# Kernel optimization log

Hardware: AMD Instinct MI355X
Metric: run time of the kernel (lower is better)

## Reference

```python
import jax, jax.numpy as jnp
import numpy as np

H = 1024      # hidden_size
V = 32000     # output_size (vocab)
L = 512       # max_length (encoder positions)
B = 256       # batch


def setup_inputs() -> dict:
    key = jax.random.key(0)
    ks = jax.random.split(key, 12)
    s = 0.02
    return {
        "input": jax.random.randint(ks[0], (B,), 0, V),
        "hidden": jax.random.normal(ks[1], (1, B, H), jnp.float32),
        "encoder_outputs": jax.random.normal(ks[2], (L, H), jnp.float32),
        # learned params (PyTorch layout: Linear weight is [out, in])
        "emb": jax.random.normal(ks[3], (V, H), jnp.float32) * s,
        "attn_W": jax.random.normal(ks[4], (L, 2 * H), jnp.float32) * s,
        "attn_b": jnp.zeros((L,), jnp.float32),
        "comb_W": jax.random.normal(ks[5], (H, 2 * H), jnp.float32) * s,
        "comb_b": jnp.zeros((H,), jnp.float32),
        "W_ih": jax.random.normal(ks[6], (3 * H, H), jnp.float32) * s,
        "W_hh": jax.random.normal(ks[7], (3 * H, H), jnp.float32) * s,
        "b_ih": jnp.zeros((3 * H,), jnp.float32),
        "b_hh": jnp.zeros((3 * H,), jnp.float32),
        "out_W": jax.random.normal(ks[8], (V, H), jnp.float32) * s,
        "out_b": jnp.zeros((V,), jnp.float32),
    }


def reference(input, hidden, encoder_outputs, emb, attn_W, attn_b,
              comb_W, comb_b, W_ih, W_hh, b_ih, b_hh, out_W, out_b):
    h = hidden[0]                                   # [B,H]
    embedded = emb[input]                           # [B,H] (dropout in eval mode = identity)
    attn_logits = jnp.concatenate([embedded, h], axis=1) @ attn_W.T + attn_b
    attn_weights = jax.nn.softmax(attn_logits, axis=1)        # [B,L]
    attn_applied = attn_weights @ encoder_outputs              # [B,H]
    x = jnp.concatenate([embedded, attn_applied], axis=1) @ comb_W.T + comb_b
    x = jax.nn.relu(x)                                         # [B,H]
    # single-step GRU (PyTorch gate layout: r, z, n)
    gi = x @ W_ih.T + b_ih                                     # [B,3H]
    gh = h @ W_hh.T + b_hh                                     # [B,3H]
    gi_r, gi_z, gi_n = jnp.split(gi, 3, axis=1)
    gh_r, gh_z, gh_n = jnp.split(gh, 3, axis=1)
    r = jax.nn.sigmoid(gi_r + gh_r)
    z = jax.nn.sigmoid(gi_z + gh_z)
    n = jnp.tanh(gi_n + r * gh_n)
    h_new = (1.0 - z) * n + z * h                              # [B,H]
    output = jax.nn.log_softmax(h_new @ out_W.T + out_b, axis=1)  # [B,V]
    return output, h_new[None], attn_weights
```

## Files before the change

kernel.cpp:

```cpp
#include <hip/hip_runtime.h>
#include <hip/hip_bf16.h>
#include <cstdint>

#define DEVI __device__ __forceinline__

typedef __bf16 bf16x8 __attribute__((ext_vector_type(8)));
typedef float  f32x4  __attribute__((ext_vector_type(4)));

constexpr int Hdim = 1024;
constexpr int Vdim = 32000;
constexpr int Ldim = 512;
constexpr int Bdim = 256;

DEVI unsigned short f2bf(float f) {
  __bf16 h = (__bf16)f;
  return __builtin_bit_cast(unsigned short, h);
}

constexpr int FP4 = 36;

__global__ __launch_bounds__(1024, 4)
void gemm_flat5(const unsigned short* __restrict__ A,
                const float* __restrict__ W,
                const float* __restrict__ bias,
                float* __restrict__ C,
                float2* __restrict__ plse)
{
  __shared__ unsigned short lW[4][128 * FP4];

  const int t    = threadIdx.x;
  const int lane = t & 63;
  const int wv   = t >> 6;
  const int r16  = lane & 15;
  const int k8   = (lane >> 4) * 8;
  const int n0   = blockIdx.x * 128;

  const int srow = t >> 3;
  const int stc  = (t & 7) * 4;

  const float*          Wb = W + (size_t)(n0 + srow) * 1024 + stc;
  const unsigned short* Ab = A + (size_t)(wv * 16 + r16) * 1024 + k8;

  f32x4 acc[8];
#pragma unroll
  for (int n = 0; n < 8; ++n)
#pragma unroll
    for (int r = 0; r < 4; ++r) acc[n][r] = 0.f;

  f32x4 w0_, w1_;
  uint4 a0_, a1_, a2_, a3_;

#define LOADW(RW, KT) RW = *reinterpret_cast<const f32x4*>(Wb + (KT) * 32)
#define LOADA(RA, KT) RA = *reinterpret_cast<const uint4*>(Ab + (KT) * 32)

#define STOREW(RW, BUF) do {                                                   \
    ushort4 u_;                                                                \
    u_.x = f2bf(RW[0]); u_.y = f2bf(RW[1]);                                    \
    u_.z = f2bf(RW[2]); u_.w = f2bf(RW[3]);                                    \
    *reinterpret_cast<ushort4*>(&lW[BUF][srow * FP4 + stc]) = u_;              \
  } while (0)

#define COMP(RA, BUF) do {                                                     \
    _Pragma("unroll")                                                          \
    for (int n = 0; n < 8; ++n) {                                              \
      bf16x8 bw_ = *reinterpret_cast<const bf16x8*>(                           \
          &lW[BUF][(n * 16 + r16) * FP4 + k8]);                                \
      acc[n] = __builtin_amdgcn_mfma_f32_16x16x32_bf16(                        \
          __builtin_bit_cast(bf16x8, RA), bw_, acc[n], 0, 0, 0);               \
    }                                                                          \
  } while (0)

  LOADW(w0_, 0); LOADW(w1_, 1);
  LOADA(a0_, 0); LOADA(a1_, 1); LOADA(a2_, 2); LOADA(a3_, 3);
  STOREW(w0_, 0); LOADW(w0_, 2);
  STOREW(w1_, 1); LOADW(w1_, 3);
  __syncthreads();

  for (int kt = 0; kt < 32; kt += 4) {
    COMP(a0_, 0);
    STOREW(w0_, 2);
    { const int kn = (kt + 4 < 32) ? kt + 4 : 31; LOADW(w0_, kn); LOADA(a0_, kn); }
    __syncthreads();

    COMP(a1_, 1);
    STOREW(w1_, 3);
    { const int kn = (kt + 5 < 32) ? kt + 5 : 31; LOADW(w1_, kn); LOADA(a1_, kn); }
    __syncthreads();

    COMP(a2_, 2);
    STOREW(w0_, 0);
    { const int kn = (kt + 6 < 32) ? kt + 6 : 31; LOADW(w0_, kn); LOADA(a2_, kn); }
    __syncthreads();

    COMP(a3_, 3);
    STOREW(w1_, 1);
    { const int kn = (kt + 7 < 32) ? kt + 7 : 31; LOADW(w1_, kn); LOADA(a3_, kn); }
    __syncthreads();
  }

#undef COMP
#undef STOREW
#undef LOADA
#undef LOADW

#pragma unroll
  for (int n = 0; n < 8; ++n) {
    const int col = n0 + n * 16 + r16;
    const float bv = bias[col];
    const int rbase = wv * 16 + (lane >> 4) * 4;
#pragma unroll
    for (int r = 0; r < 4; ++r) {
      const float v = acc[n][r] + bv;
      acc[n][r] = v;
      C[(size_t)(rbase + r) * Vdim + col] = v;
    }
  }
#pragma unroll
  for (int r = 0; r < 4; ++r) {
    float mx = -1e30f;
#pragma unroll
    for (int n = 0; n < 8; ++n) mx = fmaxf(mx, acc[n][r]);
#pragma unroll
    for (int o = 1; o < 16; o <<= 1) mx = fmaxf(mx, __shfl_xor(mx, o, 16));
    float s = 0.f;
#pragma unroll
    for (int n = 0; n < 8; ++n) s += __expf(acc[n][r] - mx);
#pragma unroll
    for (int o = 1; o < 16; o <<= 1) s += __shfl_xor(s, o, 16);
    if (r16 == 0) {
      const int row = wv * 16 + (lane >> 4) * 4 + r;
      plse[(size_t)row * gridDim.x + blockIdx.x] = make_float2(mx, s);
    }
  }
}

template<int WM, bool ABF16, bool DUAL>
__global__ __launch_bounds__(256, 2)
void gemm_bt(const void* __restrict__ Av0, const float* __restrict__ Wt0,
             const void* __restrict__ Av1, const float* __restrict__ Wt1,
             const float* __restrict__ bias,
             float* __restrict__ C0, float* __restrict__ C1,
             int K, int ldc, int col_off, int act, int aact0,
             int nsplit)
{
  constexpr int MT    = 4 * WM;
  constexpr int PITCH = 40;
  constexpr int ITA   = MT / 32;
  constexpr int MR    = WM / 16;

  __shared__ unsigned short lA[2 * MT * PITCH];
  __shared__ unsigned short lW[2 * 64 * PITCH];

  const int t  = threadIdx.x;
  const int m0 = blockIdx.y * MT;
  const int n0 = blockIdx.x * 64;

  int kz = blockIdx.z, half = 0;
  if (DUAL) { half = (kz >= nsplit) ? 1 : 0; kz -= half * nsplit; }
  const int NK = K / (32 * nsplit);
  const int kb = kz * NK;

  const void*  Av = (DUAL && half) ? Av1 : Av0;
  const float* Wt = (DUAL && half) ? Wt1 : Wt0;
  float*       C  = (DUAL && half) ? C1  : C0;
  const int  aact = (DUAL && half) ? 0 : aact0;

  const int tr = t >> 3;
  const int tc = (t & 7) * 4;

  const float*          Af = ABF16 ? nullptr : ((const float*)Av) + (size_t)m0 * K;
  const unsigned short* Ab = ABF16 ? ((const unsigned short*)Av) + (size_t)m0 * K : nullptr;
  const float*          Wb = Wt + (size_t)n0 * K;

  const int lane = t & 63;
  const int wv   = t >> 6;
  const int r16  = lane & 15;
  const int k8   = (lane >> 4) * 8;

  f32x4 acc[MR][4];
#pragma unroll
  for (int m = 0; m < MR; ++m)
#pragma unroll
    for (int n = 0; n < 4; ++n)
#pragma unroll
      for (int r = 0; r < 4; ++r) acc[m][n][r] = 0.f;

  struct RS { f32x4 ra[ITA]; ushort4 rab[ITA]; f32x4 rw[2]; };

  auto loadT = [&](RS& rg, int kt) {
    const int ko = (kb + kt) * 32 + tc;
    if constexpr (ABF16) {
      const unsigned short* ap = Ab + ko;
#pragma unroll
      for (int i = 0; i < ITA; ++i)
        rg.rab[i] = *reinterpret_cast<const ushort4*>(ap + (size_t)(tr + 32 * i) * K);
    } else {
      const float* ap = Af + ko;
#pragma unroll
      for (int i = 0; i < ITA; ++i)
        rg.ra[i] = *reinterpret_cast<const f32x4*>(ap + (size_t)(tr + 32 * i) * K);
    }
    const float* wp = Wb + ko;
#pragma unroll
    for (int i = 0; i < 2; ++i)
      rg.rw[i] = *reinterpret_cast<const f32x4*>(wp + (size_t)(tr + 32 * i) * K);
  };

  auto storeT = [&](RS& rg, int bo) {
    unsigned short* sA = &lA[bo * MT * PITCH];
    unsigned short* sW = &lW[bo * 64 * PITCH];
#pragma unroll
    for (int i = 0; i < ITA; ++i) {
      ushort4 u;
      if constexpr (ABF16) u = rg.rab[i];
      else {
        f32x4 v = rg.ra[i];
        if (aact) { v[0]=fmaxf(v[0],0.f); v[1]=fmaxf(v[1],0.f);
                    v[2]=fmaxf(v[2],0.f); v[3]=fmaxf(v[3],0.f); }
        u.x = f2bf(v[0]); u.y = f2bf(v[1]); u.z = f2bf(v[2]); u.w = f2bf(v[3]);
      }
      *reinterpret_cast<ushort4*>(&sA[(tr + 32 * i) * PITCH + tc]) = u;
    }
#pragma unroll
    for (int i = 0; i < 2; ++i) {
      f32x4 v = rg.rw[i]; ushort4 u;
      u.x = f2bf(v[0]); u.y = f2bf(v[1]); u.z = f2bf(v[2]); u.w = f2bf(v[3]);
      *reinterpret_cast<ushort4*>(&sW[(tr + 32 * i) * PITCH + tc]) = u;
    }
  };

  auto comp = [&](int bo) {
    const unsigned short* sA = &lA[bo * MT * PITCH];
    const unsigned short* sW = &lW[bo * 64 * PITCH];
    bf16x8 af[MR], bfr[4];
#pragma unroll
    for (int m = 0; m < MR; ++m)
      af[m] = *reinterpret_cast<const bf16x8*>(&sA[(wv * WM + m * 16 + r16) * PITCH + k8]);
#pragma unroll
    for (int n = 0; n < 4; ++n)
      bfr[n] = *reinterpret_cast<const bf16x8*>(&sW[(n * 16 + r16) * PITCH + k8]);
#pragma unroll
    for (int m = 0; m < MR; ++m)
#pragma unroll
      for (int n = 0; n < 4; ++n)
        acc[m][n] = __builtin_amdgcn_mfma_f32_16x16x32_bf16(af[m], bfr[n], acc[m][n], 0, 0, 0);
  };

#define GB_BARRIER() do { \
    asm volatile("s_waitcnt lgkmcnt(0)" ::: "memory"); \
    __builtin_amdgcn_sched_barrier(0); \
    __builtin_amdgcn_s_barrier(); \
  } while (0)

  RS ra_, rb_;
  loadT(ra_, 0);
  loadT(rb_, 1);
  storeT(ra_, 0);
  GB_BARRIER();

  for (int kt = 0; kt < NK; kt += 2) {
    if (kt + 2 < NK) loadT(ra_, kt + 2);
    comp(0);
    storeT(rb_, 1);
    GB_BARRIER();
    if (kt + 3 < NK) loadT(rb_, kt + 3);
    comp(1);
    if (kt + 2 < NK) {
      storeT(ra_, 0);
      GB_BARRIER();
    }
  }
#undef GB_BARRIER

#pragma unroll
  for (int n = 0; n < 4; ++n) {
    const int col = n0 + n * 16 + r16;
    const float bv = (bias && nsplit == 1) ? bias[col] : 0.f;
#pragma unroll
    for (int m = 0; m < MR; ++m) {
      const int rbase = m0 + wv * WM + m * 16 + (lane >> 4) * 4;
#pragma unroll
      for (int r = 0; r < 4; ++r) {
        float v = acc[m][n][r] + bv;
        if (act) v = fmaxf(v, 0.f);
        if (nsplit > 1) {
          atomicAdd(&C[(size_t)(rbase + r) * ldc + col_off + col], v);
        } else {
          C[(size_t)(rbase + r) * ldc + col_off + col] = v;
        }
      }
    }
  }
}

__global__ void prep_kernel(const int* __restrict__ ids, const float* __restrict__ hid,
                            const float* __restrict__ emb,
                            const float* __restrict__ attn_b, const float* __restrict__ comb_b,
                            const float* __restrict__ b_ih, const float* __restrict__ b_hh,
                            float* __restrict__ X0, float* __restrict__ X1,
                            float* __restrict__ alog, float* __restrict__ xact,
                            float* __restrict__ gi, float* __restrict__ gh)
{
  const int b = blockIdx.x, t = threadIdx.x;
  const int row = ids[b];
  f32x4 e = *reinterpret_cast<const f32x4*>(emb + (size_t)row * Hdim + t * 4);
  *reinterpret_cast<f32x4*>(X0 + (size_t)b * 2048 + t * 4) = e;
  *reinterpret_cast<f32x4*>(X1 + (size_t)b * 2048 + t * 4) = e;
  f32x4 h = *reinterpret_cast<const f32x4*>(hid + (size_t)b * Hdim + t * 4);
  *reinterpret_cast<f32x4*>(X0 + (size_t)b * 2048 + 1024 + t * 4) = h;
  f32x4 z4 = {0.f, 0.f, 0.f, 0.f};
  *reinterpret_cast<f32x4*>(X1 + (size_t)b * 2048 + 1024 + t * 4) = z4;
  if (t < 128)
    *reinterpret_cast<f32x4*>(alog + (size_t)b * Ldim + t * 4) =
        *reinterpret_cast<const f32x4*>(attn_b + t * 4);
  *reinterpret_cast<f32x4*>(xact + (size_t)b * Hdim + t * 4) =
      *reinterpret_cast<const f32x4*>(comb_b + t * 4);
#pragma unroll
  for (int i = 0; i < 3; ++i) {
    *reinterpret_cast<f32x4*>(gi + (size_t)b * 3072 + i * 1024 + t * 4) =
        *reinterpret_cast<const f32x4*>(b_ih + i * 1024 + t * 4);
    *reinterpret_cast<f32x4*>(gh + (size_t)b * 3072 + i * 1024 + t * 4) =
        *reinterpret_cast<const f32x4*>(b_hh + i * 1024 + t * 4);
  }
}

__global__ void transpose_kernel(const float* __restrict__ enc, float* __restrict__ encT)
{
  __shared__ float tile[64][65];
  const int l0 = blockIdx.x * 64, h0 = blockIdx.y * 64;
  const int t = threadIdx.x;
  const int c = t & 63, rr = t >> 6;
#pragma unroll
  for (int p = 0; p < 16; ++p) {
    const int r = p * 4 + rr;
    tile[r][c] = enc[(size_t)(l0 + r) * Hdim + h0 + c];
  }
  __syncthreads();
#pragma unroll
  for (int p = 0; p < 16; ++p) {
    const int r = p * 4 + rr;
    encT[(size_t)(h0 + r) * Ldim + l0 + c] = tile[c][r];
  }
}

__global__ void attn_softmax_kernel(const float* __restrict__ logits, float* __restrict__ wout)
{
  __shared__ float red[256];
  const int b = blockIdx.x, t = threadIdx.x;
  const float x0 = logits[b * Ldim + t];
  const float x1 = logits[b * Ldim + 256 + t];
  red[t] = fmaxf(x0, x1); __syncthreads();
  for (int o = 128; o > 0; o >>= 1) { if (t < o) red[t] = fmaxf(red[t], red[t + o]); __syncthreads(); }
  const float m = red[0]; __syncthreads();
  const float e0 = __expf(x0 - m), e1 = __expf(x1 - m);
  red[t] = e0 + e1; __syncthreads();
  for (int o = 128; o > 0; o >>= 1) { if (t < o) red[t] += red[t + o]; __syncthreads(); }
  const float inv = 1.f / red[0];
  wout[b * Ldim + t]       = e0 * inv;
  wout[b * Ldim + 256 + t] = e1 * inv;
}

DEVI float sigm(float x) { return 1.f / (1.f + __expf(-x)); }

__global__ void gru_kernel(const float* __restrict__ gi, const float* __restrict__ gh,
                           const float* __restrict__ hin,
                           float* __restrict__ hnew, unsigned short* __restrict__ hnbf)
{
  const int idx = blockIdx.x * 256 + threadIdx.x;
  const int b = idx >> 10, j = idx & 1023;
  const float* gib = gi + (size_t)b * 3072;
  const float* ghb = gh + (size_t)b * 3072;
  const float r = sigm(gib[j] + ghb[j]);
  const float z = sigm(gib[1024 + j] + ghb[1024 + j]);
  const float n = tanhf(gib[2048 + j] + r * ghb[2048 + j]);
  const float h = hin[idx];
  const float hn = (1.f - z) * n + z * h;
  hnew[idx] = hn;
  hnbf[idx] = f2bf(hn);
}

__global__ void lse_reduce(const float2* __restrict__ part, int npart,
                           float* __restrict__ lse)
{
  __shared__ float rm[256], rs[256];
  const int b = blockIdx.x, t = threadIdx.x;
  float m = -1e30f, s = 0.f;
  for (int j = t; j < npart; j += 256) {
    const float2 p = part[(size_t)b * npart + j];
    const float nm = fmaxf(m, p.x);
    s = s * __expf(m - nm) + p.y * __expf(p.x - nm);
    m = nm;
  }
  rm[t] = m; rs[t] = s; __syncthreads();
  for (int o = 128; o > 0; o >>= 1) {
    if (t < o) {
      const float m2 = rm[t + o], s2 = rs[t + o];
      const float nm = fmaxf(rm[t], m2);
      rs[t] = rs[t] * __expf(rm[t] - nm) + s2 * __expf(m2 - nm);
      rm[t] = nm;
    }
    __syncthreads();
  }
  if (t == 0) lse[b] = rm[0] + __logf(rs[0]);
}

__global__ void lsm_sub(const float* __restrict__ lse, float* __restrict__ out)
{
  const int b = blockIdx.x >> 3, c = blockIdx.x & 7;
  const float l = lse[b];
  f32x4* row4 = reinterpret_cast<f32x4*>(out + (size_t)b * Vdim) + c * 1000;
  for (int i = threadIdx.x; i < 1000; i += 256) {
    f32x4 x = row4[i];
    x[0] -= l; x[1] -= l; x[2] -= l; x[3] -= l;
    row4[i] = x;
  }
}

extern "C" void kernel_launch(void* const* d_in, const int* in_sizes, int n_in,
                              void* d_out, int out_size, void* d_ws, size_t ws_size,
                              hipStream_t stream)
{
  (void)in_sizes; (void)n_in; (void)out_size; (void)ws_size;

  const int*   ids    = (const int*)  d_in[0];
  const float* hid    = (const float*)d_in[1];
  const float* enc    = (const float*)d_in[2];
  const float* emb    = (const float*)d_in[3];
  const float* attn_W = (const float*)d_in[4];
  const float* attn_b = (const float*)d_in[5];
  const float* comb_W = (const float*)d_in[6];
  const float* comb_b = (const float*)d_in[7];
  const float* W_ih   = (const float*)d_in[8];
  const float* W_hh   = (const float*)d_in[9];
  const float* b_ih   = (const float*)d_in[10];
  const float* b_hh   = (const float*)d_in[11];
  const float* out_W  = (const float*)d_in[12];
  const float* out_b  = (const float*)d_in[13];

  float* out_logits = (float*)d_out;
  float* out_h      = out_logits + (size_t)Bdim * Vdim;
  float* out_attw   = out_h + (size_t)Bdim * Hdim;

  char* w = (char*)d_ws;
  float* X0   = (float*)w; w += (size_t)Bdim * 2048 * 4;
  float* X1   = (float*)w; w += (size_t)Bdim * 2048 * 4;
  float* encT = (float*)w; w += (size_t)Hdim * Ldim * 4;
  float* alog = (float*)w; w += (size_t)Bdim * Ldim * 4;
  float* xact = (float*)w; w += (size_t)Bdim * Hdim * 4;
  float* gi   = (float*)w; w += (size_t)Bdim * 3 * Hdim * 4;
  float* gh   = (float*)w; w += (size_t)Bdim * 3 * Hdim * 4;
  unsigned short* hnbf = (unsigned short*)w; w += (size_t)Bdim * Hdim * 2;
  float2* plse = (float2*)w; w += (size_t)Bdim * (Vdim / 32) * 8;
  float* lse  = (float*)w; w += (size_t)Bdim * 4;

  prep_kernel<<<Bdim, 256, 0, stream>>>(ids, hid, emb, attn_b, comb_b, b_ih, b_hh,
                                        X0, X1, alog, xact, gi, gh);
  transpose_kernel<<<dim3(Ldim / 64, Hdim / 64), 256, 0, stream>>>(enc, encT);

  gemm_bt<32, false, false><<<dim3(Ldim / 64, 2, 8), 256, 0, stream>>>(
      X0, attn_W, nullptr, nullptr, nullptr, alog, nullptr,
      2048, Ldim, 0, 0, 0, 8);
  attn_softmax_kernel<<<Bdim, 256, 0, stream>>>(alog, out_attw);

  gemm_bt<32, false, false><<<dim3(Hdim / 64, 2, 4), 256, 0, stream>>>(
      out_attw, encT, nullptr, nullptr, nullptr, X1, nullptr,
      512, 2048, 1024, 0, 0, 4);

  gemm_bt<32, false, false><<<dim3(Hdim / 64, 2, 8), 256, 0, stream>>>(
      X1, comb_W, nullptr, nullptr, nullptr, xact, nullptr,
      2048, Hdim, 0, 0, 0, 8);

  gemm_bt<32, false, true><<<dim3(3 * Hdim / 64, 2, 8), 256, 0, stream>>>(
      xact, W_ih, hid, W_hh, nullptr, gi, gh,
      1024, 3 * Hdim, 0, 0, 1, 4);

  gru_kernel<<<Bdim * Hdim / 256, 256, 0, stream>>>(gi, gh, hid, out_h, hnbf);

  gemm_flat5<<<Vdim / 128, 1024, 0, stream>>>(hnbf, out_W, out_b, out_logits, plse);

  lse_reduce<<<Bdim, 256, 0, stream>>>(plse, Vdim / 128, lse);
  lsm_sub<<<Bdim * 8, 256, 0, stream>>>(lse, out_logits);
}
```

Before: 122.0 us.

## Merge independent GEMMs into grouped launches and drop encoder transpose kernel

Replaces the templated split-K GEMM with a grouped kernel that takes two problem descriptors. This runs the attention-logit GEMM and the hidden-state W_hh GEMM in one launch, and moves the W_hh half out of the later dual launch. Encoder outputs are now read directly with a transposed-B load path instead of a separate transpose kernel, and the LSE reduce is fused into the log-softmax subtraction. The goal is fewer launches and less extra memory traffic. In exchange, every 8-block row group redundantly recomputes the LSE reduction, and the transposed-B LDS stores are scalar 2-byte writes that may cause bank conflicts.

```diff
diff --git a/kernel.cpp b/kernel.cpp
--- a/kernel.cpp
+++ b/kernel.cpp
@@ -134,43 +134,38 @@
   }
 }
 
-template<int WM, bool ABF16, bool DUAL>
+struct GP {
+  const float* A; const float* W; float* C;
+  int K, ldc, ldb, col_off, aact, nsplit, gx;
+};
+
+template<bool BTRANS>
 __global__ __launch_bounds__(256, 2)
-void gemm_bt(const void* __restrict__ Av0, const float* __restrict__ Wt0,
-             const void* __restrict__ Av1, const float* __restrict__ Wt1,
-             const float* __restrict__ bias,
-             float* __restrict__ C0, float* __restrict__ C1,
-             int K, int ldc, int col_off, int act, int aact0,
-             int nsplit)
-{
-  constexpr int MT    = 4 * WM;
-  constexpr int PITCH = 40;
-  constexpr int ITA   = MT / 32;
-  constexpr int MR    = WM / 16;
+void gemm_multi(GP q0, GP q1, int n0blk)
+{
+  constexpr int MT = 128, PITCH = 40, ITA = 4, MR = 2;
 
   __shared__ unsigned short lA[2 * MT * PITCH];
   __shared__ unsigned short lW[2 * 64 * PITCH];
 
+  GP p = q0;
+  int id = blockIdx.x;
+  if (id >= n0blk) { p = q1; id -= n0blk; }
+  const int bx  = id % p.gx;
+  const int rem = id / p.gx;
+  const int by  = rem & 1;
+  const int kz  = rem >> 1;
+
+  const int m0 = by * MT;
+  const int n0 = bx * 64;
+  const int NK = p.K / (32 * p.nsplit);
+  const int kb = kz * NK;
+
   const int t  = threadIdx.x;
-  const int m0 = blockIdx.y * MT;
-  const int n0 = blockIdx.x * 64;
-
-  int kz = blockIdx.z, half = 0;
-  if (DUAL) { half = (kz >= nsplit) ? 1 : 0; kz -= half * nsplit; }
-  const int NK = K / (32 * nsplit);
-  const int kb = kz * NK;
-
-  const void*  Av = (DUAL && half) ? Av1 : Av0;
-  const float* Wt = (DUAL && half) ? Wt1 : Wt0;
-  float*       C  = (DUAL && half) ? C1  : C0;
-  const int  aact = (DUAL && half) ? 0 : aact0;
-
   const int tr = t >> 3;
   const int tc = (t & 7) * 4;
 
-  const float*          Af = ABF16 ? nullptr : ((const float*)Av) + (size_t)m0 * K;
-  const unsigned short* Ab = ABF16 ? ((const unsigned short*)Av) + (size_t)m0 * K : nullptr;
-  const float*          Wb = Wt + (size_t)n0 * K;
+  const float* Af = p.A + (size_t)m0 * p.K;
 
   const int lane = t & 63;
   const int wv   = t >> 6;
@@ -185,25 +180,24 @@
 #pragma unroll
       for (int r = 0; r < 4; ++r) acc[m][n][r] = 0.f;
 
-  struct RS { f32x4 ra[ITA]; ushort4 rab[ITA]; f32x4 rw[2]; };
+  struct RS { f32x4 ra[ITA]; f32x4 rw[2]; };
 
   auto loadT = [&](RS& rg, int kt) {
-    const int ko = (kb + kt) * 32 + tc;
-    if constexpr (ABF16) {
-      const unsigned short* ap = Ab + ko;
-#pragma unroll
-      for (int i = 0; i < ITA; ++i)
-        rg.rab[i] = *reinterpret_cast<const ushort4*>(ap + (size_t)(tr + 32 * i) * K);
+    const int ko = (kb + kt) * 32;
+#pragma unroll
+    for (int i = 0; i < ITA; ++i)
+      rg.ra[i] = *reinterpret_cast<const f32x4*>(
+          Af + (size_t)(tr + 32 * i) * p.K + ko + tc);
+    if constexpr (BTRANS) {
+      const float* wp = p.W + (size_t)(ko + tr) * p.ldb + n0 + (t & 7) * 8;
+      rg.rw[0] = *reinterpret_cast<const f32x4*>(wp);
+      rg.rw[1] = *reinterpret_cast<const f32x4*>(wp + 4);
     } else {
-      const float* ap = Af + ko;
-#pragma unroll
-      for (int i = 0; i < ITA; ++i)
-        rg.ra[i] = *reinterpret_cast<const f32x4*>(ap + (size_t)(tr + 32 * i) * K);
-    }
-    const float* wp = Wb + ko;
-#pragma unroll
-    for (int i = 0; i < 2; ++i)
-      rg.rw[i] = *reinterpret_cast<const f32x4*>(wp + (size_t)(tr + 32 * i) * K);
+#pragma unroll
+      for (int i = 0; i < 2; ++i)
+        rg.rw[i] = *reinterpret_cast<const f32x4*>(
+            p.W + (size_t)(n0 + tr + 32 * i) * p.ldb + ko + tc);
+    }
   };
 
   auto storeT = [&](RS& rg, int bo) {
@@ -211,21 +205,27 @@
     unsigned short* sW = &lW[bo * 64 * PITCH];
 #pragma unroll
     for (int i = 0; i < ITA; ++i) {
+      f32x4 v = rg.ra[i];
+      if (p.aact) { v[0]=fmaxf(v[0],0.f); v[1]=fmaxf(v[1],0.f);
+                    v[2]=fmaxf(v[2],0.f); v[3]=fmaxf(v[3],0.f); }
       ushort4 u;
-      if constexpr (ABF16) u = rg.rab[i];
-      else {
-        f32x4 v = rg.ra[i];
-        if (aact) { v[0]=fmaxf(v[0],0.f); v[1]=fmaxf(v[1],0.f);
-                    v[2]=fmaxf(v[2],0.f); v[3]=fmaxf(v[3],0.f); }
+      u.x = f2bf(v[0]); u.y = f2bf(v[1]); u.z = f2bf(v[2]); u.w = f2bf(v[3]);
+      *reinterpret_cast<ushort4*>(&sA[(tr + 32 * i) * PITCH + tc]) = u;
+    }
+    if constexpr (BTRANS) {
+      const int hb = (t & 7) * 8;
+#pragma unroll
+      for (int j = 0; j < 4; ++j) {
+        sW[(hb + j)     * PITCH + tr] = f2bf(rg.rw[0][j]);
+        sW[(hb + 4 + j) * PITCH + tr] = f2bf(rg.rw[1][j]);
+      }
+    } else {
+#pragma unroll
+      for (int i = 0; i < 2; ++i) {
+        f32x4 v = rg.rw[i]; ushort4 u;
         u.x = f2bf(v[0]); u.y = f2bf(v[1]); u.z = f2bf(v[2]); u.w = f2bf(v[3]);
+        *reinterpret_cast<ushort4*>(&sW[(tr + 32 * i) * PITCH + tc]) = u;
       }
-      *reinterpret_cast<ushort4*>(&sA[(tr + 32 * i) * PITCH + tc]) = u;
-    }
-#pragma unroll
-    for (int i = 0; i < 2; ++i) {
-      f32x4 v = rg.rw[i]; ushort4 u;
-      u.x = f2bf(v[0]); u.y = f2bf(v[1]); u.z = f2bf(v[2]); u.w = f2bf(v[3]);
-      *reinterpret_cast<ushort4*>(&sW[(tr + 32 * i) * PITCH + tc]) = u;
     }
   };
 
@@ -235,7 +235,7 @@
     bf16x8 af[MR], bfr[4];
 #pragma unroll
     for (int m = 0; m < MR; ++m)
-      af[m] = *reinterpret_cast<const bf16x8*>(&sA[(wv * WM + m * 16 + r16) * PITCH + k8]);
+      af[m] = *reinterpret_cast<const bf16x8*>(&sA[(wv * 32 + m * 16 + r16) * PITCH + k8]);
 #pragma unroll
     for (int n = 0; n < 4; ++n)
       bfr[n] = *reinterpret_cast<const bf16x8*>(&sW[(n * 16 + r16) * PITCH + k8]);
@@ -275,20 +275,13 @@
 #pragma unroll
   for (int n = 0; n < 4; ++n) {
     const int col = n0 + n * 16 + r16;
-    const float bv = (bias && nsplit == 1) ? bias[col] : 0.f;
 #pragma unroll
     for (int m = 0; m < MR; ++m) {
-      const int rbase = m0 + wv * WM + m * 16 + (lane >> 4) * 4;
-#pragma unroll
-      for (int r = 0; r < 4; ++r) {
-        float v = acc[m][n][r] + bv;
-        if (act) v = fmaxf(v, 0.f);
-        if (nsplit > 1) {
-          atomicAdd(&C[(size_t)(rbase + r) * ldc + col_off + col], v);
-        } else {
-          C[(size_t)(rbase + r) * ldc + col_off + col] = v;
-        }
-      }
+      const int rbase = m0 + wv * 32 + m * 16 + (lane >> 4) * 4;
+#pragma unroll
+      for (int r = 0; r < 4; ++r)
+        atomicAdd(&p.C[(size_t)(rbase + r) * p.ldc + p.col_off + col],
+                  acc[m][n][r]);
     }
   }
 }
@@ -324,25 +317,6 @@
   }
 }
 
-__global__ void transpose_kernel(const float* __restrict__ enc, float* __restrict__ encT)
-{
-  __shared__ float tile[64][65];
-  const int l0 = blockIdx.x * 64, h0 = blockIdx.y * 64;
-  const int t = threadIdx.x;
-  const int c = t & 63, rr = t >> 6;
-#pragma unroll
-  for (int p = 0; p < 16; ++p) {
-    const int r = p * 4 + rr;
-    tile[r][c] = enc[(size_t)(l0 + r) * Hdim + h0 + c];
-  }
-  __syncthreads();
-#pragma unroll
-  for (int p = 0; p < 16; ++p) {
-    const int r = p * 4 + rr;
-    encT[(size_t)(h0 + r) * Ldim + l0 + c] = tile[c][r];
-  }
-}
-
 __global__ void attn_softmax_kernel(const float* __restrict__ logits, float* __restrict__ wout)
 {
   __shared__ float red[256];
@@ -379,11 +353,12 @@
   hnbf[idx] = f2bf(hn);
 }
 
-__global__ void lse_reduce(const float2* __restrict__ part, int npart,
-                           float* __restrict__ lse)
+__global__ void lsm_sub2(const float2* __restrict__ part, int npart,
+                         float* __restrict__ out)
 {
   __shared__ float rm[256], rs[256];
-  const int b = blockIdx.x, t = threadIdx.x;
+  const int b = blockIdx.x >> 3, c = blockIdx.x & 7;
+  const int t = threadIdx.x;
   float m = -1e30f, s = 0.f;
   for (int j = t; j < npart; j += 256) {
     const float2 p = part[(size_t)b * npart + j];
@@ -401,17 +376,11 @@
     }
     __syncthreads();
   }
-  if (t == 0) lse[b] = rm[0] + __logf(rs[0]);
-}
-
-__global__ void lsm_sub(const float* __restrict__ lse, float* __restrict__ out)
-{
-  const int b = blockIdx.x >> 3, c = blockIdx.x & 7;
-  const float l = lse[b];
+  const float lse = rm[0] + __logf(rs[0]);
   f32x4* row4 = reinterpret_cast<f32x4*>(out + (size_t)b * Vdim) + c * 1000;
-  for (int i = threadIdx.x; i < 1000; i += 256) {
+  for (int i = t; i < 1000; i += 256) {
     f32x4 x = row4[i];
-    x[0] -= l; x[1] -= l; x[2] -= l; x[3] -= l;
+    x[0] -= lse; x[1] -= lse; x[2] -= lse; x[3] -= lse;
     row4[i] = x;
   }
 }
@@ -444,40 +413,47 @@
   char* w = (char*)d_ws;
   float* X0   = (float*)w; w += (size_t)Bdim * 2048 * 4;
   float* X1   = (float*)w; w += (size_t)Bdim * 2048 * 4;
-  float* encT = (float*)w; w += (size_t)Hdim * Ldim * 4;
   float* alog = (float*)w; w += (size_t)Bdim * Ldim * 4;
   float* xact = (float*)w; w += (size_t)Bdim * Hdim * 4;
   float* gi   = (float*)w; w += (size_t)Bdim * 3 * Hdim * 4;
   float* gh   = (float*)w; w += (size_t)Bdim * 3 * Hdim * 4;
   unsigned short* hnbf = (unsigned short*)w; w += (size_t)Bdim * Hdim * 2;
-  float2* plse = (float2*)w; w += (size_t)Bdim * (Vdim / 32) * 8;
-  float* lse  = (float*)w; w += (size_t)Bdim * 4;
+  float2* plse = (float2*)w; w += (size_t)Bdim * (Vdim / 128) * 8;
 
   prep_kernel<<<Bdim, 256, 0, stream>>>(ids, hid, emb, attn_b, comb_b, b_ih, b_hh,
                                         X0, X1, alog, xact, gi, gh);
-  transpose_kernel<<<dim3(Ldim / 64, Hdim / 64), 256, 0, stream>>>(enc, encT);
-
-  gemm_bt<32, false, false><<<dim3(Ldim / 64, 2, 8), 256, 0, stream>>>(
-      X0, attn_W, nullptr, nullptr, nullptr, alog, nullptr,
-      2048, Ldim, 0, 0, 0, 8);
+
+  {
+    GP p0 = { X0,  attn_W, alog, 2048, Ldim,     2048, 0, 0, 8,  Ldim / 64 };
+    GP p1 = { hid, W_hh,   gh,   1024, 3 * Hdim, 1024, 0, 0, 4,  3 * Hdim / 64 };
+    const int n0blk = p0.gx * 2 * p0.nsplit;
+    const int nblk  = n0blk + p1.gx * 2 * p1.nsplit;
+    gemm_multi<false><<<nblk, 256, 0, stream>>>(p0, p1, n0blk);
+  }
+
   attn_softmax_kernel<<<Bdim, 256, 0, stream>>>(alog, out_attw);
 
-  gemm_bt<32, false, false><<<dim3(Hdim / 64, 2, 4), 256, 0, stream>>>(
-      out_attw, encT, nullptr, nullptr, nullptr, X1, nullptr,
-      512, 2048, 1024, 0, 0, 4);
-
-  gemm_bt<32, false, false><<<dim3(Hdim / 64, 2, 8), 256, 0, stream>>>(
-      X1, comb_W, nullptr, nullptr, nullptr, xact, nullptr,
-      2048, Hdim, 0, 0, 0, 8);
-
-  gemm_bt<32, false, true><<<dim3(3 * Hdim / 64, 2, 8), 256, 0, stream>>>(
-      xact, W_ih, hid, W_hh, nullptr, gi, gh,
-      1024, 3 * Hdim, 0, 0, 1, 4);
+  {
+    GP p0 = { out_attw, enc, X1, 512, 2048, Hdim, 1024, 0, 4, Hdim / 64 };
+    const int nblk = p0.gx * 2 * p0.nsplit;
+    gemm_multi<true><<<nblk, 256, 0, stream>>>(p0, p0, nblk);
+  }
+
+  {
+    GP p0 = { X1, comb_W, xact, 2048, Hdim, 2048, 0, 0, 8, Hdim / 64 };
+    const int nblk = p0.gx * 2 * p0.nsplit;
+    gemm_multi<false><<<nblk, 256, 0, stream>>>(p0, p0, nblk);
+  }
+
+  {
+    GP p0 = { xact, W_ih, gi, 1024, 3 * Hdim, 1024, 0, 1, 4, 3 * Hdim / 64 };
+    const int nblk = p0.gx * 2 * p0.nsplit;
+    gemm_multi<false><<<nblk, 256, 0, stream>>>(p0, p0, nblk);
+  }
 
   gru_kernel<<<Bdim * Hdim / 256, 256, 0, stream>>>(gi, gh, hid, out_h, hnbf);
 
   gemm_flat5<<<Vdim / 128, 1024, 0, stream>>>(hnbf, out_W, out_b, out_logits, plse);
 
-  lse_reduce<<<Bdim, 256, 0, stream>>>(plse, Vdim / 128, lse);
-  lsm_sub<<<Bdim * 8, 256, 0, stream>>>(lse, out_logits);
-}
+  lsm_sub2<<<Bdim * 8, 256, 0, stream>>>(plse, Vdim / 128, out_logits);
+}
```

Measured after the change: 115.6 us. 5.3% less time.
